# Kernel tuning notes

Hardware: AMD Instinct MI355X
Metric: run time of the kernel (lower is better)

## Reference

```python
import jax, jax.numpy as jnp
import numpy as np

N, D = 16384, 2048


def setup_inputs() -> dict:
    key = jax.random.key(0)
    k1, k2 = jax.random.split(key)
    x = jax.random.normal(k1, (N, D), dtype=jnp.float32)
    mask = jax.random.randint(k2, (N, D), 0, 2) > 0
    return {"x": x, "mask": mask}


def _masked_sparsemax(z, m):
    """Project each row of z onto the simplex restricted to positions where m is True.

    Fully batched equivalent of the TF per-row map_fn/cond/boolean_mask version.
    z: [..., D] float, m: [..., D] bool. Returns p with p>=0, sum over active = 1
    (all-zeros row if no active entries).
    """
    d = z.shape[-1]
    num_active = jnp.sum(m, axis=-1, keepdims=True)                 # [..., 1] int
    # Masked entries sort to the tail (-inf), so the first num_active sorted
    # entries are exactly the active values in descending order.
    z_neg = jnp.where(m, z, -jnp.inf)
    z_sorted = -jnp.sort(-z_neg, axis=-1)                           # descending
    k_int = jnp.arange(1, d + 1)
    k = k_int.astype(z.dtype)
    active_pos = k_int <= num_active                                # [..., D]
    # cumsum over active sorted entries only (zeros beyond num_active)
    csum = jnp.cumsum(jnp.where(active_pos, z_sorted, 0.0), axis=-1)
    # support condition: z_(k) - (csum_k - 1)/k > 0  <=>  k*z_(k) > csum_k - 1
    cond = (z_sorted * k > (csum - 1.0)) & active_pos
    rho = jnp.sum(cond, axis=-1, keepdims=True)                     # support size
    rho_idx = jnp.clip(rho - 1, 0, d - 1)
    csum_rho = jnp.take_along_axis(csum, rho_idx, axis=-1)
    theta = (csum_rho - 1.0) / jnp.maximum(rho, 1).astype(z.dtype)
    p_valid = jnp.maximum(z - theta, 0.0)
    # TF invalid_branch fallback: uniform over active entries (unreachable in
    # exact arithmetic since k=1 always satisfies cond, kept for faithfulness)
    p_uniform = 1.0 / jnp.maximum(num_active, 1).astype(z.dtype)
    p = jnp.where(rho > 0, p_valid, p_uniform)
    return jnp.where(m & (num_active > 0), p, 0.0)


def reference(x, mask):
    # axis = -1: project along the last axis (the TF layer transposes the
    # chosen axis to last; with axis=-1 that transpose is the identity).
    return _masked_sparsemax(x, mask)
```

## Files before the change

### kernel.cpp

```cpp
#include <hip/hip_runtime.h>
#include <math.h>


constexpr int D    = 2048;
constexpr int WPB  = 4;
constexpr int TPB  = WPB * 64;
constexpr int EPT  = D / 64;
constexpr int CHK  = EPT / 4;

typedef float f4 __attribute__((ext_vector_type(4)));
typedef int   i4 __attribute__((ext_vector_type(4)));

__global__ __launch_bounds__(TPB) void sparsemax_kernel(
    const float* __restrict__ x,
    const int*   __restrict__ mask,
    float*       __restrict__ out,
    int n_rows)
{
    const int wave = threadIdx.x >> 6;
    const int lane = threadIdx.x & 63;
    const int row  = blockIdx.x * WPB + wave;
    if (row >= n_rows) return;

    const size_t rbase = (size_t)row * D;

    float z[EPT];
    #pragma unroll
    for (int c = 0; c < CHK; ++c) {
        const size_t off = rbase + (size_t)(c * 256 + lane * 4);
        const f4 a = __builtin_nontemporal_load((const f4*)(x    + off));
        const i4 m = __builtin_nontemporal_load((const i4*)(mask + off));
        z[c * 4 + 0] = m.x ? a.x : -INFINITY;
        z[c * 4 + 1] = m.y ? a.y : -INFINITY;
        z[c * 4 + 2] = m.z ? a.z : -INFINITY;
        z[c * 4 + 3] = m.w ? a.w : -INFINITY;
    }

    float m0 = z[0], m1 = z[1], m2 = z[2], m3 = z[3];
    #pragma unroll
    for (int k = 4; k < EPT; k += 4) {
        m0 = fmaxf(m0, z[k + 0]);
        m1 = fmaxf(m1, z[k + 1]);
        m2 = fmaxf(m2, z[k + 2]);
        m3 = fmaxf(m3, z[k + 3]);
    }
    float gmax = fmaxf(fmaxf(m0, m1), fmaxf(m2, m3));
    #pragma unroll
    for (int off = 32; off > 0; off >>= 1)
        gmax = fmaxf(gmax, __shfl_xor(gmax, off, 64));

    float theta;
    if (gmax == -INFINITY) {
        theta = INFINITY;
    } else {
        theta = gmax - 1.0f;
        int prevC = -1;
        for (int it = 0; it < 64; ++it) {
            float f0 = 0.0f, f1 = 0.0f, f2 = 0.0f, f3 = 0.0f;
            #pragma unroll
            for (int k = 0; k < EPT; k += 4) {
                f0 += fmaxf(z[k + 0] - theta, 0.0f);
                f1 += fmaxf(z[k + 1] - theta, 0.0f);
                f2 += fmaxf(z[k + 2] - theta, 0.0f);
                f3 += fmaxf(z[k + 3] - theta, 0.0f);
            }
            float f = (f0 + f1) + (f2 + f3);
            int C = 0;
            #pragma unroll
            for (int k = 0; k < EPT; ++k)
                C += (int)__popcll(__ballot(z[k] > theta));
            #pragma unroll
            for (int off = 32; off > 0; off >>= 1)
                f += __shfl_xor(f, off, 64);

            if (C == 0) break;
            if (C == prevC) break;
            theta += (f - 1.0f) / (float)C;
            prevC = C;
        }
    }

    #pragma unroll
    for (int c = 0; c < CHK; ++c) {
        const size_t off = rbase + (size_t)(c * 256 + lane * 4);
        float4 o;
        o.x = fmaxf(z[c * 4 + 0] - theta, 0.0f);
        o.y = fmaxf(z[c * 4 + 1] - theta, 0.0f);
        o.z = fmaxf(z[c * 4 + 2] - theta, 0.0f);
        o.w = fmaxf(z[c * 4 + 3] - theta, 0.0f);
        *(float4*)(out + off) = o;
    }
}

extern "C" void kernel_launch(void* const* d_in, const int* in_sizes, int n_in,
                              void* d_out, int out_size, void* d_ws, size_t ws_size,
                              hipStream_t stream) {
    const float* x    = (const float*)d_in[0];
    const int*   mask = (const int*)  d_in[1];
    float*       out  = (float*)d_out;
    const int n_rows = in_sizes[0] / D;
    const int blocks = (n_rows + WPB - 1) / WPB;
    sparsemax_kernel<<<blocks, TPB, 0, stream>>>(x, mask, out, n_rows);
}
```

Baseline: 296.1 us.

## Persistent waves process several rows with register prefetch of next row

Each wave now loops over about four rows with a grid stride, and it loads the next row's x and mask into registers while it computes the current row's sparsemax threshold. This is meant to hide global-load latency behind the iterative threshold computation. In exchange the grid is four times smaller and each thread holds 64 more registers for the prefetch buffers, which could lower occupancy.

```diff
diff --git a/kernel.cpp b/kernel.cpp
--- a/kernel.cpp
+++ b/kernel.cpp
@@ -3,10 +3,10 @@
 
 
 constexpr int D    = 2048;
-constexpr int WPB  = 4;
-constexpr int TPB  = WPB * 64;
+constexpr int TPB  = 256;
 constexpr int EPT  = D / 64;
 constexpr int CHK  = EPT / 4;
+constexpr int RPW  = 4;
 
 typedef float f4 __attribute__((ext_vector_type(4)));
 typedef int   i4 __attribute__((ext_vector_type(4)));
@@ -15,80 +15,108 @@
     const float* __restrict__ x,
     const int*   __restrict__ mask,
     float*       __restrict__ out,
-    int n_rows)
+    int n_rows, int wstride)
 {
     const int wave = threadIdx.x >> 6;
     const int lane = threadIdx.x & 63;
-    const int row  = blockIdx.x * WPB + wave;
+    int row = blockIdx.x * (TPB / 64) + wave;
     if (row >= n_rows) return;
 
-    const size_t rbase = (size_t)row * D;
+    const int lo4 = lane * 4;
 
-    float z[EPT];
-    #pragma unroll
-    for (int c = 0; c < CHK; ++c) {
-        const size_t off = rbase + (size_t)(c * 256 + lane * 4);
-        const f4 a = __builtin_nontemporal_load((const f4*)(x    + off));
-        const i4 m = __builtin_nontemporal_load((const i4*)(mask + off));
-        z[c * 4 + 0] = m.x ? a.x : -INFINITY;
-        z[c * 4 + 1] = m.y ? a.y : -INFINITY;
-        z[c * 4 + 2] = m.z ? a.z : -INFINITY;
-        z[c * 4 + 3] = m.w ? a.w : -INFINITY;
-    }
-
-    float m0 = z[0], m1 = z[1], m2 = z[2], m3 = z[3];
-    #pragma unroll
-    for (int k = 4; k < EPT; k += 4) {
-        m0 = fmaxf(m0, z[k + 0]);
-        m1 = fmaxf(m1, z[k + 1]);
-        m2 = fmaxf(m2, z[k + 2]);
-        m3 = fmaxf(m3, z[k + 3]);
-    }
-    float gmax = fmaxf(fmaxf(m0, m1), fmaxf(m2, m3));
-    #pragma unroll
-    for (int off = 32; off > 0; off >>= 1)
-        gmax = fmaxf(gmax, __shfl_xor(gmax, off, 64));
-
-    float theta;
-    if (gmax == -INFINITY) {
-        theta = INFINITY;
-    } else {
-        theta = gmax - 1.0f;
-        int prevC = -1;
-        for (int it = 0; it < 64; ++it) {
-            float f0 = 0.0f, f1 = 0.0f, f2 = 0.0f, f3 = 0.0f;
-            #pragma unroll
-            for (int k = 0; k < EPT; k += 4) {
-                f0 += fmaxf(z[k + 0] - theta, 0.0f);
-                f1 += fmaxf(z[k + 1] - theta, 0.0f);
-                f2 += fmaxf(z[k + 2] - theta, 0.0f);
-                f3 += fmaxf(z[k + 3] - theta, 0.0f);
-            }
-            float f = (f0 + f1) + (f2 + f3);
-            int C = 0;
-            #pragma unroll
-            for (int k = 0; k < EPT; ++k)
-                C += (int)__popcll(__ballot(z[k] > theta));
-            #pragma unroll
-            for (int off = 32; off > 0; off >>= 1)
-                f += __shfl_xor(f, off, 64);
-
-            if (C == 0) break;
-            if (C == prevC) break;
-            theta += (f - 1.0f) / (float)C;
-            prevC = C;
+    f4 xb[CHK]; i4 mb[CHK];
+    {
+        const size_t rb = (size_t)row * D;
+        #pragma unroll
+        for (int c = 0; c < CHK; ++c) {
+            const size_t off = rb + (size_t)(c * 256 + lo4);
+            xb[c] = __builtin_nontemporal_load((const f4*)(x    + off));
+            mb[c] = __builtin_nontemporal_load((const i4*)(mask + off));
         }
     }
 
-    #pragma unroll
-    for (int c = 0; c < CHK; ++c) {
-        const size_t off = rbase + (size_t)(c * 256 + lane * 4);
-        float4 o;
-        o.x = fmaxf(z[c * 4 + 0] - theta, 0.0f);
-        o.y = fmaxf(z[c * 4 + 1] - theta, 0.0f);
-        o.z = fmaxf(z[c * 4 + 2] - theta, 0.0f);
-        o.w = fmaxf(z[c * 4 + 3] - theta, 0.0f);
-        *(float4*)(out + off) = o;
+    for (;;) {
+        const int nrow = row + wstride;
+
+        float z[EPT];
+        #pragma unroll
+        for (int c = 0; c < CHK; ++c) {
+            z[c * 4 + 0] = mb[c].x ? xb[c].x : -INFINITY;
+            z[c * 4 + 1] = mb[c].y ? xb[c].y : -INFINITY;
+            z[c * 4 + 2] = mb[c].z ? xb[c].z : -INFINITY;
+            z[c * 4 + 3] = mb[c].w ? xb[c].w : -INFINITY;
+        }
+
+        if (nrow < n_rows) {
+            const size_t rb = (size_t)nrow * D;
+            #pragma unroll
+            for (int c = 0; c < CHK; ++c) {
+                const size_t off = rb + (size_t)(c * 256 + lo4);
+                xb[c] = __builtin_nontemporal_load((const f4*)(x    + off));
+                mb[c] = __builtin_nontemporal_load((const i4*)(mask + off));
+            }
+        }
+
+        float m0 = z[0], m1 = z[1], m2 = z[2], m3 = z[3];
+        #pragma unroll
+        for (int k = 4; k < EPT; k += 4) {
+            m0 = fmaxf(m0, z[k + 0]);
+            m1 = fmaxf(m1, z[k + 1]);
+            m2 = fmaxf(m2, z[k + 2]);
+            m3 = fmaxf(m3, z[k + 3]);
+        }
+        float gmax = fmaxf(fmaxf(m0, m1), fmaxf(m2, m3));
+        #pragma unroll
+        for (int off = 32; off > 0; off >>= 1)
+            gmax = fmaxf(gmax, __shfl_xor(gmax, off, 64));
+
+        float theta;
+        if (gmax == -INFINITY) {
+            theta = INFINITY;
+        } else {
+            theta = gmax - 1.0f;
+            int prevC = -1;
+            for (int it = 0; it < 64; ++it) {
+                float f0 = 0.0f, f1 = 0.0f, f2 = 0.0f, f3 = 0.0f;
+                #pragma unroll
+                for (int k = 0; k < EPT; k += 4) {
+                    f0 += fmaxf(z[k + 0] - theta, 0.0f);
+                    f1 += fmaxf(z[k + 1] - theta, 0.0f);
+                    f2 += fmaxf(z[k + 2] - theta, 0.0f);
+                    f3 += fmaxf(z[k + 3] - theta, 0.0f);
+                }
+                float f = (f0 + f1) + (f2 + f3);
+                int C = 0;
+                #pragma unroll
+                for (int k = 0; k < EPT; ++k)
+                    C += (int)__popcll(__ballot(z[k] > theta));
+                #pragma unroll
+                for (int off = 32; off > 0; off >>= 1)
+                    f += __shfl_xor(f, off, 64);
+
+                if (C == 0) break;
+                if (C == prevC) break;
+                theta += (f - 1.0f) / (float)C;
+                prevC = C;
+            }
+        }
+
+        {
+            const size_t rb = (size_t)row * D;
+            #pragma unroll
+            for (int c = 0; c < CHK; ++c) {
+                const size_t off = rb + (size_t)(c * 256 + lo4);
+                float4 o;
+                o.x = fmaxf(z[c * 4 + 0] - theta, 0.0f);
+                o.y = fmaxf(z[c * 4 + 1] - theta, 0.0f);
+                o.z = fmaxf(z[c * 4 + 2] - theta, 0.0f);
+                o.w = fmaxf(z[c * 4 + 3] - theta, 0.0f);
+                *(float4*)(out + off) = o;
+            }
+        }
+
+        if (nrow >= n_rows) break;
+        row = nrow;
     }
 }
 
@@ -99,6 +127,8 @@
     const int*   mask = (const int*)  d_in[1];
     float*       out  = (float*)d_out;
     const int n_rows = in_sizes[0] / D;
-    const int blocks = (n_rows + WPB - 1) / WPB;
-    sparsemax_kernel<<<blocks, TPB, 0, stream>>>(x, mask, out, n_rows);
+    int n_waves = (n_rows + RPW - 1) / RPW;
+    int blocks  = (n_waves + (TPB / 64) - 1) / (TPB / 64);
+    int wstride = blocks * (TPB / 64);
+    sparsemax_kernel<<<blocks, TPB, 0, stream>>>(x, mask, out, n_rows, wstride);
 }
```

New measurement: 300.3 us. No clear change (+1.4%).
